# Kernel optimization log

Hardware: AMD Instinct MI355X
Metric: run time of the kernel (lower is better)

The kernel has to match this reference:

```python
import jax, jax.numpy as jnp
import numpy as np

N = 100_000   # nodes
E = 1_600_000 # edges
G = 512       # graphs in batch
DIN, DF, DOUT = 78, 32, 128
BN_EPS = 1e-5

def setup_inputs() -> dict:
    key = jax.random.key(0)
    ks = jax.random.split(key, 10)
    s = 0.1
    return {
        "x": jax.random.normal(ks[0], (N, DIN), jnp.float32),
        "edge_index": jax.random.randint(ks[1], (2, E), 0, N, dtype=jnp.int32),
        "batch": jnp.sort(jax.random.randint(ks[2], (N,), 0, G, dtype=jnp.int32)),
        "w1_in": jax.random.normal(ks[3], (DIN, DF), jnp.float32) * s,
        "b1_in": jnp.zeros((DF,), jnp.float32),
        "w1_out": jax.random.normal(ks[4], (DF, DF), jnp.float32) * s,
        "b1_out": jnp.zeros((DF,), jnp.float32),
        "wa": jax.random.normal(ks[5], (4, DF, DF), jnp.float32) * s,
        "ba": jnp.zeros((4, DF), jnp.float32),
        "wb": jax.random.normal(ks[6], (4, DF, DF), jnp.float32) * s,
        "bb": jnp.zeros((4, DF), jnp.float32),
        "gamma": jnp.ones((5, DF), jnp.float32),
        "beta": jnp.zeros((5, DF), jnp.float32),
        "fc_w": jax.random.normal(ks[7], (DF, DOUT), jnp.float32) * s,
        "fc_b": jnp.zeros((DOUT,), jnp.float32),
    }

def _gin_conv(h, src, dst, w1, bv1, w2, bv2):
    # GINConv with eps=0: nn(x + sum_{j in N(i)} x_j)
    agg = jax.ops.segment_sum(h[src], dst, num_segments=N)
    z = h + agg
    return jax.nn.relu(z @ w1 + bv1) @ w2 + bv2

def _bn(h, g, b):
    # BatchNorm1d, training-mode batch statistics (biased variance)
    mu = h.mean(axis=0)
    var = ((h - mu) ** 2).mean(axis=0)
    return g * (h - mu) * jax.lax.rsqrt(var + BN_EPS) + b

def reference(x, edge_index, batch, w1_in, b1_in, w1_out, b1_out,
              wa, ba, wb, bb, gamma, beta, fc_w, fc_b):
    src, dst = edge_index[0], edge_index[1]
    h = _bn(jax.nn.relu(_gin_conv(x, src, dst, w1_in, b1_in, w1_out, b1_out)), gamma[0], beta[0])
    for i in range(4):  # conv2..conv5 (identical shapes)
        h = _bn(jax.nn.relu(_gin_conv(h, src, dst, wa[i], ba[i], wb[i], bb[i])), gamma[i + 1], beta[i + 1])
    pooled = jax.ops.segment_sum(h, batch, num_segments=G)  # global_add_pool -> [G, DF]
    out = jax.nn.relu(pooled @ fc_w + fc_b)
    # dropout omitted (deterministic reference / eval semantics)
    return out
```

## Files before the change

### kernel.cpp

```cpp
#include <hip/hip_runtime.h>
#include <hip/hip_bf16.h>
#include <hip/hip_fp16.h>

#define NN 100000
#define EE 1600000
#define GG 512
#define DIN 78
#define DF 32
#define DOUT 128
#define BN_EPS 1e-5f

#define NBLK_NODE 3125

#define BSH 9
#define NBUCK 196
#define SCB 256
#define EPB (EE / SCB)

__device__ __forceinline__ unsigned short f2h(float f) {
    return __half_as_ushort(__float2half(f));
}
__device__ __forceinline__ float hlo(unsigned int v) {
    return __half2float(__ushort_as_half((unsigned short)(v & 0xFFFFu)));
}
__device__ __forceinline__ float hhi(unsigned int v) {
    return __half2float(__ushort_as_half((unsigned short)(v >> 16)));
}

__global__ __launch_bounds__(256) void k_bhist(const int* __restrict__ dst, int* __restrict__ hist_g) {
    __shared__ int hist[NBUCK];
    int tid = threadIdx.x, blk = blockIdx.x;
    if (tid < NBUCK) hist[tid] = 0;
    __syncthreads();
    int start = blk * EPB, end = start + EPB;
    for (int i = start + tid; i < end; i += 256) atomicAdd(&hist[dst[i] >> BSH], 1);
    __syncthreads();
    if (tid < NBUCK) hist_g[tid * SCB + blk] = hist[tid];
}

__global__ __launch_bounds__(256) void k_bscan(int* __restrict__ hist_g, int* __restrict__ bbase) {
    __shared__ int tot[256];
    int t = threadIdx.x;
    int total = 0;
    if (t < NBUCK)
        for (int blk = 0; blk < SCB; ++blk) total += hist_g[t * SCB + blk];
    tot[t] = (t < NBUCK) ? total : 0;
    __syncthreads();
    for (int off = 1; off < 256; off <<= 1) {
        int u = (t >= off) ? tot[t - off] : 0;
        __syncthreads();
        tot[t] += u;
        __syncthreads();
    }
    int excl = tot[t] - total;
    if (t < NBUCK) {
        bbase[t] = excl;
        int run = excl;
        for (int blk = 0; blk < SCB; ++blk) {
            int h = hist_g[t * SCB + blk];
            hist_g[t * SCB + blk] = run;
            run += h;
        }
    }
    if (t == 0) bbase[NBUCK] = EE;
}

__global__ __launch_bounds__(256) void k_bscatter(const int* __restrict__ src, const int* __restrict__ dst,
                                                  const int* __restrict__ hist_g, int* __restrict__ pairs) {
    __shared__ int base_l[NBUCK];
    __shared__ int cnt[NBUCK];
    int tid = threadIdx.x, blk = blockIdx.x;
    if (tid < NBUCK) { base_l[tid] = hist_g[tid * SCB + blk]; cnt[tid] = 0; }
    __syncthreads();
    int start = blk * EPB, end = start + EPB;
    for (int i = start + tid; i < end; i += 256) {
        int d = dst[i], s = src[i];
        int b = d >> BSH;
        int rk = atomicAdd(&cnt[b], 1);
        pairs[base_l[b] + rk] = s | ((d & 511) << 17);
    }
}

__global__ __launch_bounds__(256) void k_bfill(const int* __restrict__ pairs, const int* __restrict__ bbase,
                                               int* __restrict__ row_ptr, int* __restrict__ col) {
    __shared__ int cnt[512];
    __shared__ int excl[512];
    __shared__ int ps[256];
    int tid = threadIdx.x, b = blockIdx.x;
    int base = bbase[b];
    int cntb = bbase[b + 1] - base;
    int nbase = b << BSH;
    int nloc = NN - nbase; if (nloc > 512) nloc = 512;
    cnt[tid] = 0; cnt[tid + 256] = 0;
    __syncthreads();
    for (int i = tid; i < cntb; i += 256) atomicAdd(&cnt[(unsigned)pairs[base + i] >> 17], 1);
    __syncthreads();
    int a0 = cnt[2 * tid], a1 = cnt[2 * tid + 1];
    ps[tid] = a0 + a1;
    __syncthreads();
    for (int off = 1; off < 256; off <<= 1) {
        int u = (tid >= off) ? ps[tid - off] : 0;
        __syncthreads();
        ps[tid] += u;
        __syncthreads();
    }
    int pexcl = ps[tid] - (a0 + a1);
    excl[2 * tid] = pexcl;
    excl[2 * tid + 1] = pexcl + a0;
    __syncthreads();
    for (int i = tid; i < nloc; i += 256) row_ptr[nbase + i] = base + excl[i];
    if (b == 0 && tid == 0) row_ptr[NN] = EE;
    __syncthreads();
    for (int i = tid; i < cntb; i += 256) {
        int v = pairs[base + i];
        int dloc = (unsigned)v >> 17;
        int s = v & 0x1FFFF;
        int lp = atomicAdd(&excl[dloc], 1);
        col[base + lp] = s;
    }
}

__global__ __launch_bounds__(256) void k_proj_first(const float* __restrict__ x,
                                                    const float* __restrict__ w1,
                                                    float* __restrict__ p,
                                                    unsigned short* __restrict__ pb) {
    __shared__ float w[DIN][DF];
    __shared__ float hx[32][DIN];
    int tid = threadIdx.x;
    for (int i = tid; i < DIN * DF; i += 256) w[i >> 5][i & 31] = w1[i];
    int base = blockIdx.x * 32;
    for (int i = tid; i < 32 * DIN; i += 256) hx[i / DIN][i % DIN] = x[base * DIN + i];
    __syncthreads();
    int j = tid & 31;
    #pragma unroll
    for (int it = 0; it < 4; ++it) {
        int rown = (tid >> 5) + 8 * it;
        float acc = 0.f;
        #pragma unroll
        for (int k = 0; k < DIN; ++k) acc += hx[rown][k] * w[k][j];
        p[(base + rown) * DF + j] = acc;
        pb[(base + rown) * DF + j] = f2h(acc);
    }
}

__global__ __launch_bounds__(256) void k_proj_hidden(const float* __restrict__ r,
                                                     const float* __restrict__ w1_,
                                                     const float* __restrict__ statsL,
                                                     const float* __restrict__ gamma,
                                                     const float* __restrict__ beta,
                                                     float* __restrict__ p,
                                                     unsigned short* __restrict__ pb) {
    __shared__ float w[DF][DF];
    __shared__ float h[32][DF + 1];
    int tid = threadIdx.x;
    for (int i = tid; i < DF * DF; i += 256) w[i >> 5][i & 31] = w1_[i];
    int grp = tid >> 3, c = tid & 7;
    int node = blockIdx.x * 32 + grp;
    const float invN = 1.0f / (float)NN;
    float4 s1v = ((const float4*)statsL)[c];
    float4 s2v = ((const float4*)(statsL + DF))[c];
    float4 gv  = ((const float4*)gamma)[c];
    float4 bv  = ((const float4*)beta)[c];
    float4 rv  = ((const float4*)r)[node * 8 + c];
    float mux = s1v.x * invN, muy = s1v.y * invN, muz = s1v.z * invN, muw = s1v.w * invN;
    float ivx = rsqrtf(s2v.x * invN - mux * mux + BN_EPS);
    float ivy = rsqrtf(s2v.y * invN - muy * muy + BN_EPS);
    float ivz = rsqrtf(s2v.z * invN - muz * muz + BN_EPS);
    float ivw = rsqrtf(s2v.w * invN - muw * muw + BN_EPS);
    h[grp][4 * c + 0] = gv.x * (rv.x - mux) * ivx + bv.x;
    h[grp][4 * c + 1] = gv.y * (rv.y - muy) * ivy + bv.y;
    h[grp][4 * c + 2] = gv.z * (rv.z - muz) * ivz + bv.z;
    h[grp][4 * c + 3] = gv.w * (rv.w - muw) * ivw + bv.w;
    __syncthreads();
    int j = tid & 31;
    #pragma unroll
    for (int it = 0; it < 4; ++it) {
        int rown = (tid >> 5) + 8 * it;
        float acc = 0.f;
        #pragma unroll
        for (int k = 0; k < DF; ++k) acc += h[rown][k] * w[k][j];
        p[(blockIdx.x * 32 + rown) * DF + j] = acc;
        pb[(blockIdx.x * 32 + rown) * DF + j] = f2h(acc);
    }
}

__global__ __launch_bounds__(256) void k_agg(const float* __restrict__ p,
                                             const unsigned short* __restrict__ pb,
                                             const int* __restrict__ row_ptr,
                                             const int* __restrict__ col,
                                             const float* __restrict__ b1,
                                             const float* __restrict__ w2_,
                                             const float* __restrict__ b2,
                                             float* __restrict__ r,
                                             float* __restrict__ statsL) {
    __shared__ float w[DF][DF];
    __shared__ float a[32][DF + 1];
    __shared__ float red[4][2][DF];
    int tid = threadIdx.x;
    for (int i = tid; i < DF * DF; i += 256) w[i >> 5][i & 31] = w2_[i];
    int grp = tid >> 3, c = tid & 7;
    int base = blockIdx.x * 32;
    int node = base + grp;
    const float4* p4 = (const float4*)p;
    const uint2* pb2 = (const uint2*)pb;
    float4 b1v = ((const float4*)b1)[c];
    float4 self = p4[node * 8 + c];
    float4 acc0, acc1, acc2, acc3;
    acc0.x = self.x + b1v.x; acc0.y = self.y + b1v.y;
    acc0.z = self.z + b1v.z; acc0.w = self.w + b1v.w;
    acc1.x = acc1.y = acc1.z = acc1.w = 0.f;
    acc2.x = acc2.y = acc2.z = acc2.w = 0.f;
    acc3.x = acc3.y = acc3.z = acc3.w = 0.f;
    int e0 = row_ptr[node], e1 = row_ptr[node + 1];
    int e = e0;
    for (; e + 4 <= e1; e += 4) {
        int s0 = col[e], s1 = col[e + 1], s2 = col[e + 2], s3 = col[e + 3];
        uint2 q0 = pb2[s0 * 8 + c];
        uint2 q1 = pb2[s1 * 8 + c];
        uint2 q2 = pb2[s2 * 8 + c];
        uint2 q3 = pb2[s3 * 8 + c];
        acc0.x += hlo(q0.x); acc0.y += hhi(q0.x); acc0.z += hlo(q0.y); acc0.w += hhi(q0.y);
        acc1.x += hlo(q1.x); acc1.y += hhi(q1.x); acc1.z += hlo(q1.y); acc1.w += hhi(q1.y);
        acc2.x += hlo(q2.x); acc2.y += hhi(q2.x); acc2.z += hlo(q2.y); acc2.w += hhi(q2.y);
        acc3.x += hlo(q3.x); acc3.y += hhi(q3.x); acc3.z += hlo(q3.y); acc3.w += hhi(q3.y);
    }
    for (; e < e1; ++e) {
        uint2 q = pb2[col[e] * 8 + c];
        acc0.x += hlo(q.x); acc0.y += hhi(q.x); acc0.z += hlo(q.y); acc0.w += hhi(q.y);
    }
    acc0.x += acc1.x + acc2.x + acc3.x;
    acc0.y += acc1.y + acc2.y + acc3.y;
    acc0.z += acc1.z + acc2.z + acc3.z;
    acc0.w += acc1.w + acc2.w + acc3.w;
    a[grp][4 * c + 0] = fmaxf(acc0.x, 0.f);
    a[grp][4 * c + 1] = fmaxf(acc0.y, 0.f);
    a[grp][4 * c + 2] = fmaxf(acc0.z, 0.f);
    a[grp][4 * c + 3] = fmaxf(acc0.w, 0.f);
    __syncthreads();
    int j = tid & 31;
    float b2j = b2[j];
    float s1 = 0.f, s2 = 0.f;
    #pragma unroll
    for (int it = 0; it < 4; ++it) {
        int rown = (tid >> 5) + 8 * it;
        float accm = b2j;
        #pragma unroll
        for (int k = 0; k < DF; ++k) accm += a[rown][k] * w[k][j];
        float rv = fmaxf(accm, 0.f);
        r[(base + rown) * DF + j] = rv;
        s1 += rv;
        s2 += rv * rv;
    }
    s1 += __shfl_down(s1, 32);
    s2 += __shfl_down(s2, 32);
    int wave = tid >> 6, lane = tid & 63;
    if (lane < 32) { red[wave][0][j] = s1; red[wave][1][j] = s2; }
    __syncthreads();
    if (tid < 32) {
        float t1 = red[0][0][j] + red[1][0][j] + red[2][0][j] + red[3][0][j];
        float t2 = red[0][1][j] + red[1][1][j] + red[2][1][j] + red[3][1][j];
        atomicAdd(&statsL[j], t1);
        atomicAdd(&statsL[DF + j], t2);
    }
}

__global__ __launch_bounds__(256) void k_pool(const float* __restrict__ r,
                                              const float* __restrict__ statsL,
                                              const float* __restrict__ gamma,
                                              const float* __restrict__ beta,
                                              const int* __restrict__ batch,
                                              float* __restrict__ pooled) {
    int t = blockIdx.x * 256 + threadIdx.x;
    int nodeBase = (t >> 5) * 8;
    if (nodeBase >= NN) return;
    int j = t & 31;
    const float invN = 1.0f / (float)NN;
    float mu = statsL[j] * invN;
    float inv = rsqrtf(statsL[DF + j] * invN - mu * mu + BN_EPS);
    float gj = gamma[j], bj = beta[j];
    float accp = 0.f;
    int curg = batch[nodeBase];
    #pragma unroll
    for (int k = 0; k < 8; ++k) {
        int n = nodeBase + k;
        int g = batch[n];
        float val = gj * (r[n * DF + j] - mu) * inv + bj;
        if (g != curg) { atomicAdd(&pooled[curg * DF + j], accp); accp = 0.f; curg = g; }
        accp += val;
    }
    atomicAdd(&pooled[curg * DF + j], accp);
}

__global__ __launch_bounds__(128) void k_fc(const float* __restrict__ pooled,
                                            const float* __restrict__ fc_w,
                                            const float* __restrict__ fc_b,
                                            float* __restrict__ out) {
    __shared__ float pl[DF];
    int g = blockIdx.x, j = threadIdx.x;
    if (j < DF) pl[j] = pooled[g * DF + j];
    __syncthreads();
    float acc = fc_b[j];
    #pragma unroll
    for (int k = 0; k < DF; ++k) acc += pl[k] * fc_w[k * DOUT + j];
    out[g * DOUT + j] = fmaxf(acc, 0.f);
}

extern "C" void kernel_launch(void* const* d_in, const int* in_sizes, int n_in,
                              void* d_out, int out_size, void* d_ws, size_t ws_size,
                              hipStream_t stream) {
    const float* x      = (const float*)d_in[0];
    const int*   eidx   = (const int*)d_in[1];
    const int*   batch  = (const int*)d_in[2];
    const float* w1_in  = (const float*)d_in[3];
    const float* b1_in  = (const float*)d_in[4];
    const float* w1_out = (const float*)d_in[5];
    const float* b1_out = (const float*)d_in[6];
    const float* wa     = (const float*)d_in[7];
    const float* ba     = (const float*)d_in[8];
    const float* wb     = (const float*)d_in[9];
    const float* bb     = (const float*)d_in[10];
    const float* gamma  = (const float*)d_in[11];
    const float* beta   = (const float*)d_in[12];
    const float* fc_w   = (const float*)d_in[13];
    const float* fc_b   = (const float*)d_in[14];
    float* out = (float*)d_out;

    const int* esrc = eidx;
    const int* edst = eidx + EE;

    float* W = (float*)d_ws;
    float* p       = W;
    float* r       = p + (size_t)NN * DF;
    float* pooled  = r + (size_t)NN * DF;
    float* stats   = pooled + (size_t)GG * DF;
    int* row_ptr = (int*)(stats + 5 * 64);
    int* col     = row_ptr + (NN + 1);
    int* hist_g  = col + EE;
    int* bbase   = hist_g + NBUCK * SCB;
    unsigned short* pb = (unsigned short*)(bbase + NBUCK + 1);
    int* pairs   = (int*)p;

    k_bhist<<<SCB, 256, 0, stream>>>(edst, hist_g);
    k_bscan<<<1, 256, 0, stream>>>(hist_g, bbase);
    k_bscatter<<<SCB, 256, 0, stream>>>(esrc, edst, hist_g, pairs);
    k_bfill<<<NBUCK, 256, 0, stream>>>(pairs, bbase, row_ptr, col);

    hipMemsetAsync(stats, 0, sizeof(float) * 5 * 64, stream);

    k_proj_first<<<NBLK_NODE, 256, 0, stream>>>(x, w1_in, p, pb);
    k_agg<<<NBLK_NODE, 256, 0, stream>>>(p, pb, row_ptr, col, b1_in, w1_out, b1_out, r, stats);

    for (int i = 1; i < 5; ++i) {
        const float* w1_ = wa + (size_t)(i - 1) * DF * DF;
        const float* b1_ = ba + (size_t)(i - 1) * DF;
        const float* w2_ = wb + (size_t)(i - 1) * DF * DF;
        const float* b2_ = bb + (size_t)(i - 1) * DF;
        const float* g_  = gamma + (size_t)(i - 1) * DF;
        const float* be_ = beta + (size_t)(i - 1) * DF;
        k_proj_hidden<<<NBLK_NODE, 256, 0, stream>>>(r, w1_, stats + (i - 1) * 64, g_, be_, p, pb);
        k_agg<<<NBLK_NODE, 256, 0, stream>>>(p, pb, row_ptr, col, b1_, w2_, b2_, r, stats + i * 64);
    }

    hipMemsetAsync(pooled, 0, sizeof(float) * GG * DF, stream);
    k_pool<<<((NN / 8) * 32 + 255) / 256, 256, 0, stream>>>(r, stats + 4 * 64, gamma + 4 * DF,
                                                            beta + 4 * DF, batch, pooled);
    k_fc<<<GG, 128, 0, stream>>>(pooled, fc_w, fc_b, out);
}
```

Measured before the change: 801.8 us.

## Partition neighbor lists by source quarter and sync blocks between gather phases

The CSR build now sorts each node's neighbors into four ranges by source index (source >> 15) and stores the per-quarter counts packed in a new qoff array. The aggregation kernel walks the four ranges in turn, with a block barrier between them. The aim is to keep the gathered source rows in a narrower address window at any moment so they stay in cache. The cost is extra barriers, extra LDS atomics and scanning in the fill kernel, and per-node degree counts that must fit in 8 bits per quarter.

After: 822.6 us. 2.6% more time.

```diff
diff --git a/kernel.cpp b/kernel.cpp
--- a/kernel.cpp
+++ b/kernel.cpp
@@ -82,21 +82,29 @@
 }
 
 __global__ __launch_bounds__(256) void k_bfill(const int* __restrict__ pairs, const int* __restrict__ bbase,
-                                               int* __restrict__ row_ptr, int* __restrict__ col) {
-    __shared__ int cnt[512];
-    __shared__ int excl[512];
+                                               int* __restrict__ row_ptr, int* __restrict__ qoff,
+                                               int* __restrict__ col) {
+    __shared__ int c4[2048];
+    __shared__ int nstart[512];
     __shared__ int ps[256];
     int tid = threadIdx.x, b = blockIdx.x;
     int base = bbase[b];
     int cntb = bbase[b + 1] - base;
     int nbase = b << BSH;
     int nloc = NN - nbase; if (nloc > 512) nloc = 512;
-    cnt[tid] = 0; cnt[tid + 256] = 0;
-    __syncthreads();
-    for (int i = tid; i < cntb; i += 256) atomicAdd(&cnt[(unsigned)pairs[base + i] >> 17], 1);
-    __syncthreads();
-    int a0 = cnt[2 * tid], a1 = cnt[2 * tid + 1];
-    ps[tid] = a0 + a1;
+    for (int i = tid; i < 2048; i += 256) c4[i] = 0;
+    __syncthreads();
+    for (int i = tid; i < cntb; i += 256) {
+        int v = pairs[base + i];
+        int dloc = (unsigned)v >> 17;
+        int q = (v & 0x1FFFF) >> 15;
+        atomicAdd(&c4[dloc * 4 + q], 1);
+    }
+    __syncthreads();
+    int n0 = 2 * tid, n1 = 2 * tid + 1;
+    int t0 = c4[n0 * 4] + c4[n0 * 4 + 1] + c4[n0 * 4 + 2] + c4[n0 * 4 + 3];
+    int t1 = c4[n1 * 4] + c4[n1 * 4 + 1] + c4[n1 * 4 + 2] + c4[n1 * 4 + 3];
+    ps[tid] = t0 + t1;
     __syncthreads();
     for (int off = 1; off < 256; off <<= 1) {
         int u = (tid >= off) ? ps[tid - off] : 0;
@@ -104,18 +112,31 @@
         ps[tid] += u;
         __syncthreads();
     }
-    int pexcl = ps[tid] - (a0 + a1);
-    excl[2 * tid] = pexcl;
-    excl[2 * tid + 1] = pexcl + a0;
-    __syncthreads();
-    for (int i = tid; i < nloc; i += 256) row_ptr[nbase + i] = base + excl[i];
+    int pexcl = ps[tid] - (t0 + t1);
+    nstart[n0] = pexcl;
+    nstart[n1] = pexcl + t0;
+    #pragma unroll
+    for (int kk = 0; kk < 2; ++kk) {
+        int n = (kk == 0) ? n0 : n1;
+        if (n < nloc) {
+            int s = nstart[n];
+            int c0 = c4[n * 4], c1 = c4[n * 4 + 1], c2 = c4[n * 4 + 2];
+            c4[n * 4]     = s;
+            c4[n * 4 + 1] = s + c0;
+            c4[n * 4 + 2] = s + c0 + c1;
+            c4[n * 4 + 3] = s + c0 + c1 + c2;
+            row_ptr[nbase + n] = base + s;
+            qoff[nbase + n] = c0 | (c1 << 8) | (c2 << 16);
+        }
+    }
     if (b == 0 && tid == 0) row_ptr[NN] = EE;
     __syncthreads();
     for (int i = tid; i < cntb; i += 256) {
         int v = pairs[base + i];
         int dloc = (unsigned)v >> 17;
         int s = v & 0x1FFFF;
-        int lp = atomicAdd(&excl[dloc], 1);
+        int q = s >> 15;
+        int lp = atomicAdd(&c4[dloc * 4 + q], 1);
         col[base + lp] = s;
     }
 }
@@ -187,6 +208,7 @@
 __global__ __launch_bounds__(256) void k_agg(const float* __restrict__ p,
                                              const unsigned short* __restrict__ pb,
                                              const int* __restrict__ row_ptr,
+                                             const int* __restrict__ qoff,
                                              const int* __restrict__ col,
                                              const float* __restrict__ b1,
                                              const float* __restrict__ w2_,
@@ -212,22 +234,37 @@
     acc2.x = acc2.y = acc2.z = acc2.w = 0.f;
     acc3.x = acc3.y = acc3.z = acc3.w = 0.f;
     int e0 = row_ptr[node], e1 = row_ptr[node + 1];
-    int e = e0;
-    for (; e + 4 <= e1; e += 4) {
-        int s0 = col[e], s1 = col[e + 1], s2 = col[e + 2], s3 = col[e + 3];
-        uint2 q0 = pb2[s0 * 8 + c];
-        uint2 q1 = pb2[s1 * 8 + c];
-        uint2 q2 = pb2[s2 * 8 + c];
-        uint2 q3 = pb2[s3 * 8 + c];
-        acc0.x += hlo(q0.x); acc0.y += hhi(q0.x); acc0.z += hlo(q0.y); acc0.w += hhi(q0.y);
-        acc1.x += hlo(q1.x); acc1.y += hhi(q1.x); acc1.z += hlo(q1.y); acc1.w += hhi(q1.y);
-        acc2.x += hlo(q2.x); acc2.y += hhi(q2.x); acc2.z += hlo(q2.y); acc2.w += hhi(q2.y);
-        acc3.x += hlo(q3.x); acc3.y += hhi(q3.x); acc3.z += hlo(q3.y); acc3.w += hhi(q3.y);
-    }
-    for (; e < e1; ++e) {
-        uint2 q = pb2[col[e] * 8 + c];
-        acc0.x += hlo(q.x); acc0.y += hhi(q.x); acc0.z += hlo(q.y); acc0.w += hhi(q.y);
-    }
+    int qc = qoff[node];
+    int q1 = e0 + (qc & 255);
+    int q2 = q1 + ((qc >> 8) & 255);
+    int q3 = q2 + ((qc >> 16) & 255);
+
+    auto walk = [&](int s, int t) {
+        int e = s;
+        for (; e + 4 <= t; e += 4) {
+            int s0 = col[e], s1 = col[e + 1], s2 = col[e + 2], s3 = col[e + 3];
+            uint2 v0 = pb2[s0 * 8 + c];
+            uint2 v1 = pb2[s1 * 8 + c];
+            uint2 v2 = pb2[s2 * 8 + c];
+            uint2 v3 = pb2[s3 * 8 + c];
+            acc0.x += hlo(v0.x); acc0.y += hhi(v0.x); acc0.z += hlo(v0.y); acc0.w += hhi(v0.y);
+            acc1.x += hlo(v1.x); acc1.y += hhi(v1.x); acc1.z += hlo(v1.y); acc1.w += hhi(v1.y);
+            acc2.x += hlo(v2.x); acc2.y += hhi(v2.x); acc2.z += hlo(v2.y); acc2.w += hhi(v2.y);
+            acc3.x += hlo(v3.x); acc3.y += hhi(v3.x); acc3.z += hlo(v3.y); acc3.w += hhi(v3.y);
+        }
+        for (; e < t; ++e) {
+            uint2 v = pb2[col[e] * 8 + c];
+            acc0.x += hlo(v.x); acc0.y += hhi(v.x); acc0.z += hlo(v.y); acc0.w += hhi(v.y);
+        }
+    };
+    walk(e0, q1);
+    __syncthreads();
+    walk(q1, q2);
+    __syncthreads();
+    walk(q2, q3);
+    __syncthreads();
+    walk(q3, e1);
+
     acc0.x += acc1.x + acc2.x + acc3.x;
     acc0.y += acc1.y + acc2.y + acc3.y;
     acc0.z += acc1.z + acc2.z + acc3.z;
@@ -338,17 +375,18 @@
     int* hist_g  = col + EE;
     int* bbase   = hist_g + NBUCK * SCB;
     unsigned short* pb = (unsigned short*)(bbase + NBUCK + 1);
+    int* qoff    = (int*)(pb + (size_t)NN * DF);
     int* pairs   = (int*)p;
 
     k_bhist<<<SCB, 256, 0, stream>>>(edst, hist_g);
     k_bscan<<<1, 256, 0, stream>>>(hist_g, bbase);
     k_bscatter<<<SCB, 256, 0, stream>>>(esrc, edst, hist_g, pairs);
-    k_bfill<<<NBUCK, 256, 0, stream>>>(pairs, bbase, row_ptr, col);
+    k_bfill<<<NBUCK, 256, 0, stream>>>(pairs, bbase, row_ptr, qoff, col);
 
     hipMemsetAsync(stats, 0, sizeof(float) * 5 * 64, stream);
 
     k_proj_first<<<NBLK_NODE, 256, 0, stream>>>(x, w1_in, p, pb);
-    k_agg<<<NBLK_NODE, 256, 0, stream>>>(p, pb, row_ptr, col, b1_in, w1_out, b1_out, r, stats);
+    k_agg<<<NBLK_NODE, 256, 0, stream>>>(p, pb, row_ptr, qoff, col, b1_in, w1_out, b1_out, r, stats);
 
     for (int i = 1; i < 5; ++i) {
         const float* w1_ = wa + (size_t)(i - 1) * DF * DF;
@@ -358,7 +396,7 @@
         const float* g_  = gamma + (size_t)(i - 1) * DF;
         const float* be_ = beta + (size_t)(i - 1) * DF;
         k_proj_hidden<<<NBLK_NODE, 256, 0, stream>>>(r, w1_, stats + (i - 1) * 64, g_, be_, p, pb);
-        k_agg<<<NBLK_NODE, 256, 0, stream>>>(p, pb, row_ptr, col, b1_, w2_, b2_, r, stats + i * 64);
+        k_agg<<<NBLK_NODE, 256, 0, stream>>>(p, pb, row_ptr, qoff, col, b1_, w2_, b2_, r, stats + i * 64);
     }
 
     hipMemsetAsync(pooled, 0, sizeof(float) * GG * DF, stream);
```
